# Performance work log

Hardware: AMD Instinct MI355X
Metric: run time of the kernel (lower is better)

The kernel has to match this reference:

```python
import jax, jax.numpy as jnp
import numpy as np

TAU_1 = 100.0


def setup_inputs() -> dict:
    key = jax.random.key(0)
    z = jax.random.normal(key, (8192, 512), dtype=jnp.float32)
    return {"z": z}


def reference(z) -> jnp.ndarray:
    # InfoNCE_l2 variant: log E_{i!=j}[ exp(-||z_i - z_j||^2 / tau_1) ]
    N = z.shape[0]
    sq = jnp.sum(z * z, axis=1)                      # [N]
    # squared euclidean distances: ||zi||^2 + ||zj||^2 - 2 zi.zj, clamped at 0
    D = jnp.maximum(sq[:, None] + sq[None, :] - 2.0 * (z @ z.T), 0.0)  # [N, N]
    E = jnp.exp(-D / TAU_1)
    # zero out the diagonal, average over the N*(N-1) off-diagonal entries
    off_diag_sum = jnp.sum(E) - jnp.sum(jnp.diagonal(E))
    mean_off = off_diag_sum / (N * (N - 1))
    return jnp.log(mean_off)
```

## Files before the change

kernel.cpp:

```cpp
#include <hip/hip_runtime.h>
#include <hip/hip_bf16.h>

#define NROWS 8192
#define KDIM  512
#define NT    64
#define NBLK  (NT*(NT+1)/2)
#define SCL1  0x7F7F7F7F
#define STRIP_BYTES (32 * KDIM)
#define C2    0.0144269504f

typedef __attribute__((ext_vector_type(16))) float f32x16;
typedef __attribute__((ext_vector_type(4))) int i32x4;
typedef __attribute__((ext_vector_type(8))) int i32x8;

__device__ __forceinline__ i32x8 mk_op(i32x4 lo, i32x4 hi) {
    i32x8 r;
    r[0] = lo[0]; r[1] = lo[1]; r[2] = lo[2]; r[3] = lo[3];
    r[4] = hi[0]; r[5] = hi[1]; r[6] = hi[2]; r[7] = hi[3];
    return r;
}

__global__ __launch_bounds__(256) void prep_kernel(const float* __restrict__ z,
                                                   unsigned char* __restrict__ zb2,
                                                   float* __restrict__ nq) {
    int wave = threadIdx.x >> 6, lane = threadIdx.x & 63;
    int row = blockIdx.x * 4 + wave;
    const float* zr = z + (size_t)row * KDIM + lane * 8;
    float4 v0 = *(const float4*)zr;
    float4 v1 = *(const float4*)(zr + 4);
    float vals[8] = {v0.x, v0.y, v0.z, v0.w, v1.x, v1.y, v1.z, v1.w};
    float s = 0.f;
#pragma unroll
    for (int i = 0; i < 8; ++i) s += vals[i] * vals[i];
    int lo = __builtin_amdgcn_cvt_pk_fp8_f32(vals[0], vals[1], 0, false);
    lo     = __builtin_amdgcn_cvt_pk_fp8_f32(vals[2], vals[3], lo, true);
    int hi = __builtin_amdgcn_cvt_pk_fp8_f32(vals[4], vals[5], 0, false);
    hi     = __builtin_amdgcn_cvt_pk_fp8_f32(vals[6], vals[7], hi, true);
    int2 pk; pk.x = lo; pk.y = hi;
    int strip = row >> 5, lr = row & 31;
    size_t addr = (size_t)strip * STRIP_BYTES + (lane >> 3) * 2048 +
                  ((lane >> 1) & 3) * 512 + lr * 16 + (lane & 1) * 8;
    *(int2*)(zb2 + addr) = pk;
#pragma unroll
    for (int off = 32; off; off >>= 1) s += __shfl_down(s, off);
    if (lane == 0) nq[row] = -C2 * s;
}

__global__ __launch_bounds__(256, 2) void gram_kernel(const unsigned char* __restrict__ zb2,
                                                      const float* __restrict__ nq,
                                                      float* __restrict__ part) {
    __shared__ float wsum[4];

    int tid = threadIdx.x;
    int wave = tid >> 6, lane = tid & 63;
    int ln31 = lane & 31, kh = lane >> 5;
    int wm = wave >> 1, wn = wave & 1;

    int rem = blockIdx.x, bi = 0;
    while (rem >= NT - bi) { rem -= NT - bi; ++bi; }
    int bj = bi + rem;
    int rot = blockIdx.x & 7;

    int sA = bi * 4 + wm * 2;
    int sB = bj * 4 + wn * 2;
    int laneOff = kh * 1024 + ln31 * 16;
    const unsigned char* pA0 = zb2 + (size_t)sA * STRIP_BYTES + laneOff;
    const unsigned char* pA1 = pA0 + STRIP_BYTES;
    const unsigned char* pB0 = zb2 + (size_t)sB * STRIP_BYTES + laneOff;
    const unsigned char* pB1 = pB0 + STRIP_BYTES;

    f32x16 accf[2][2];
#pragma unroll
    for (int mi = 0; mi < 2; ++mi)
#pragma unroll
        for (int ni = 0; ni < 2; ++ni)
#pragma unroll
            for (int r = 0; r < 16; ++r) accf[mi][ni][r] = 0.f;

#pragma unroll
    for (int h = 0; h < 2; ++h) {
        i32x4 Av[16], Bv[16];
#pragma unroll
        for (int ks = 0; ks < 4; ++ks) {
            int off = (((h * 4 + ks + rot) & 7)) * 2048;
            Av[ks * 4 + 0] = *(const i32x4*)(pA0 + off);
            Av[ks * 4 + 1] = *(const i32x4*)(pA0 + off + 512);
            Av[ks * 4 + 2] = *(const i32x4*)(pA1 + off);
            Av[ks * 4 + 3] = *(const i32x4*)(pA1 + off + 512);
            Bv[ks * 4 + 0] = *(const i32x4*)(pB0 + off);
            Bv[ks * 4 + 1] = *(const i32x4*)(pB0 + off + 512);
            Bv[ks * 4 + 2] = *(const i32x4*)(pB1 + off);
            Bv[ks * 4 + 3] = *(const i32x4*)(pB1 + off + 512);
        }
#pragma unroll
        for (int ks = 0; ks < 4; ++ks) {
            i32x8 a0 = mk_op(Av[ks * 4 + 0], Av[ks * 4 + 1]);
            i32x8 a1 = mk_op(Av[ks * 4 + 2], Av[ks * 4 + 3]);
            i32x8 b0 = mk_op(Bv[ks * 4 + 0], Bv[ks * 4 + 1]);
            i32x8 b1 = mk_op(Bv[ks * 4 + 2], Bv[ks * 4 + 3]);
            accf[0][0] = __builtin_amdgcn_mfma_scale_f32_32x32x64_f8f6f4(a0, b0, accf[0][0], 0, 0, 0, SCL1, 0, SCL1);
            accf[0][1] = __builtin_amdgcn_mfma_scale_f32_32x32x64_f8f6f4(a0, b1, accf[0][1], 0, 0, 0, SCL1, 0, SCL1);
            accf[1][0] = __builtin_amdgcn_mfma_scale_f32_32x32x64_f8f6f4(a1, b0, accf[1][0], 0, 0, 0, SCL1, 0, SCL1);
            accf[1][1] = __builtin_amdgcn_mfma_scale_f32_32x32x64_f8f6f4(a1, b1, accf[1][1], 0, 0, 0, SCL1, 0, SCL1);
        }
    }

    int rowBase = bi * 128 + wm * 64;
    int colBase = bj * 128 + wn * 64;
    float nqj[2] = { nq[colBase + ln31], nq[colBase + 32 + ln31] };

    float local = 0.f;
    if (bi != bj) {
#pragma unroll
        for (int mi = 0; mi < 2; ++mi) {
#pragma unroll
            for (int reg = 0; reg < 16; ++reg) {
                int rowf = (reg & 3) + 8 * (reg >> 2) + 4 * kh;
                float nqi = nq[rowBase + mi * 32 + rowf];
#pragma unroll
                for (int ni = 0; ni < 2; ++ni) {
                    float arg = fmaf(accf[mi][ni][reg], 2.f * C2, nqi + nqj[ni]);
                    local += __builtin_exp2f(fminf(arg, 0.f));
                }
            }
        }
    } else {
#pragma unroll
        for (int mi = 0; mi < 2; ++mi) {
#pragma unroll
            for (int reg = 0; reg < 16; ++reg) {
                int rowf = (reg & 3) + 8 * (reg >> 2) + 4 * kh;
                int gi = rowBase + mi * 32 + rowf;
                float nqi = nq[gi];
#pragma unroll
                for (int ni = 0; ni < 2; ++ni) {
                    int gj = colBase + ni * 32 + ln31;
                    float arg = fmaf(accf[mi][ni][reg], 2.f * C2, nqi + nqj[ni]);
                    float e = __builtin_exp2f(fminf(arg, 0.f));
                    local += (gi < gj) ? e : 0.f;
                }
            }
        }
    }

#pragma unroll
    for (int off = 32; off; off >>= 1) local += __shfl_down(local, off);
    if (lane == 0) wsum[wave] = local;
    __syncthreads();
    if (tid == 0) part[blockIdx.x] = wsum[0] + wsum[1] + wsum[2] + wsum[3];
}

__global__ __launch_bounds__(256) void reduce_kernel(const float* __restrict__ part,
                                                     float* __restrict__ out) {
    int tid = threadIdx.x;
    int wave = tid >> 6, lane = tid & 63;
    float s = 0.f;
    for (int i = tid; i < NBLK; i += 256) s += part[i];
#pragma unroll
    for (int off = 32; off; off >>= 1) s += __shfl_down(s, off);
    __shared__ float w[4];
    if (lane == 0) w[wave] = s;
    __syncthreads();
    if (tid == 0) {
        float total = 2.f * (w[0] + w[1] + w[2] + w[3]);
        out[0] = logf(total / ((float)NROWS * (float)(NROWS - 1)));
    }
}

extern "C" void kernel_launch(void* const* d_in, const int* in_sizes, int n_in,
                              void* d_out, int out_size, void* d_ws, size_t ws_size,
                              hipStream_t stream) {
    const float* z = (const float*)d_in[0];
    float* out = (float*)d_out;
    unsigned char* zb2 = (unsigned char*)d_ws;
    float* nq = (float*)((char*)d_ws + (size_t)NROWS * KDIM);
    float* part = nq + NROWS;

    prep_kernel<<<NROWS / 4, 256, 0, stream>>>(z, zb2, nq);
    gram_kernel<<<NBLK, 256, 0, stream>>>(zb2, nq, part);
    reduce_kernel<<<1, 256, 0, stream>>>(part, out);
}
```

Before: 91.84 us.

## Fuse prep, gram and reduce into one persistent cooperative kernel

Replaces three launches with a single cooperative kernel of 512 persistent blocks. The blocks first quantize rows to fp8 and compute norms, then grid-sync, loop over triangular tiles, grid-sync again, and let block 0 do the final reduction. The K loop is split into four smaller halves to cut register pressure. This removes launch gaps and tail effects, but adds two grid-wide barriers and the cost of cooperative launch, and the fixed grid may balance work unevenly across the 2080 tiles.

```diff
diff --git a/kernel.cpp b/kernel.cpp
--- a/kernel.cpp
+++ b/kernel.cpp
@@ -1,10 +1,14 @@
 #include <hip/hip_runtime.h>
+#include <hip/hip_cooperative_groups.h>
 #include <hip/hip_bf16.h>
+
+namespace cg = cooperative_groups;
 
 #define NROWS 8192
 #define KDIM  512
 #define NT    64
 #define NBLK  (NT*(NT+1)/2)
+#define GRID  512
 #define SCL1  0x7F7F7F7F
 #define STRIP_BYTES (32 * KDIM)
 #define C2    0.0144269504f
@@ -20,124 +24,129 @@
     return r;
 }
 
-__global__ __launch_bounds__(256) void prep_kernel(const float* __restrict__ z,
-                                                   unsigned char* __restrict__ zb2,
-                                                   float* __restrict__ nq) {
-    int wave = threadIdx.x >> 6, lane = threadIdx.x & 63;
-    int row = blockIdx.x * 4 + wave;
-    const float* zr = z + (size_t)row * KDIM + lane * 8;
-    float4 v0 = *(const float4*)zr;
-    float4 v1 = *(const float4*)(zr + 4);
-    float vals[8] = {v0.x, v0.y, v0.z, v0.w, v1.x, v1.y, v1.z, v1.w};
-    float s = 0.f;
-#pragma unroll
-    for (int i = 0; i < 8; ++i) s += vals[i] * vals[i];
-    int lo = __builtin_amdgcn_cvt_pk_fp8_f32(vals[0], vals[1], 0, false);
-    lo     = __builtin_amdgcn_cvt_pk_fp8_f32(vals[2], vals[3], lo, true);
-    int hi = __builtin_amdgcn_cvt_pk_fp8_f32(vals[4], vals[5], 0, false);
-    hi     = __builtin_amdgcn_cvt_pk_fp8_f32(vals[6], vals[7], hi, true);
-    int2 pk; pk.x = lo; pk.y = hi;
-    int strip = row >> 5, lr = row & 31;
-    size_t addr = (size_t)strip * STRIP_BYTES + (lane >> 3) * 2048 +
-                  ((lane >> 1) & 3) * 512 + lr * 16 + (lane & 1) * 8;
-    *(int2*)(zb2 + addr) = pk;
-#pragma unroll
-    for (int off = 32; off; off >>= 1) s += __shfl_down(s, off);
-    if (lane == 0) nq[row] = -C2 * s;
-}
-
-__global__ __launch_bounds__(256, 2) void gram_kernel(const unsigned char* __restrict__ zb2,
-                                                      const float* __restrict__ nq,
-                                                      float* __restrict__ part) {
+__global__ __launch_bounds__(256, 2) void fused_kernel(const float* __restrict__ z,
+                                                       unsigned char* __restrict__ zb2,
+                                                       float* __restrict__ nq,
+                                                       float* __restrict__ part,
+                                                       float* __restrict__ out) {
+    cg::grid_group gg = cg::this_grid();
     __shared__ float wsum[4];
 
     int tid = threadIdx.x;
     int wave = tid >> 6, lane = tid & 63;
+
+#pragma unroll
+    for (int rr = 0; rr < 4; ++rr) {
+        int row = blockIdx.x * 16 + wave * 4 + rr;
+        const float* zr = z + (size_t)row * KDIM + lane * 8;
+        float4 v0 = *(const float4*)zr;
+        float4 v1 = *(const float4*)(zr + 4);
+        float vals[8] = {v0.x, v0.y, v0.z, v0.w, v1.x, v1.y, v1.z, v1.w};
+        float s = 0.f;
+#pragma unroll
+        for (int i = 0; i < 8; ++i) s += vals[i] * vals[i];
+        int lo = __builtin_amdgcn_cvt_pk_fp8_f32(vals[0], vals[1], 0, false);
+        lo     = __builtin_amdgcn_cvt_pk_fp8_f32(vals[2], vals[3], lo, true);
+        int hi = __builtin_amdgcn_cvt_pk_fp8_f32(vals[4], vals[5], 0, false);
+        hi     = __builtin_amdgcn_cvt_pk_fp8_f32(vals[6], vals[7], hi, true);
+        int2 pk; pk.x = lo; pk.y = hi;
+        int strip = row >> 5, lr = row & 31;
+        size_t addr = (size_t)strip * STRIP_BYTES + (lane >> 3) * 2048 +
+                      ((lane >> 1) & 3) * 512 + lr * 16 + (lane & 1) * 8;
+        *(int2*)(zb2 + addr) = pk;
+#pragma unroll
+        for (int off = 32; off; off >>= 1) s += __shfl_down(s, off);
+        if (lane == 0) nq[row] = -C2 * s;
+    }
+
+    __threadfence();
+    gg.sync();
+
     int ln31 = lane & 31, kh = lane >> 5;
     int wm = wave >> 1, wn = wave & 1;
+    int laneOff = kh * 1024 + ln31 * 16;
 
-    int rem = blockIdx.x, bi = 0;
-    while (rem >= NT - bi) { rem -= NT - bi; ++bi; }
-    int bj = bi + rem;
-    int rot = blockIdx.x & 7;
+    float local = 0.f;
+    for (int t = blockIdx.x; t < NBLK; t += GRID) {
+        int rem = t, bi = 0;
+        while (rem >= NT - bi) { rem -= NT - bi; ++bi; }
+        int bj = bi + rem;
+        int rot = t & 7;
 
-    int sA = bi * 4 + wm * 2;
-    int sB = bj * 4 + wn * 2;
-    int laneOff = kh * 1024 + ln31 * 16;
-    const unsigned char* pA0 = zb2 + (size_t)sA * STRIP_BYTES + laneOff;
-    const unsigned char* pA1 = pA0 + STRIP_BYTES;
-    const unsigned char* pB0 = zb2 + (size_t)sB * STRIP_BYTES + laneOff;
-    const unsigned char* pB1 = pB0 + STRIP_BYTES;
+        const unsigned char* pA0 = zb2 + (size_t)(bi * 4 + wm * 2) * STRIP_BYTES + laneOff;
+        const unsigned char* pA1 = pA0 + STRIP_BYTES;
+        const unsigned char* pB0 = zb2 + (size_t)(bj * 4 + wn * 2) * STRIP_BYTES + laneOff;
+        const unsigned char* pB1 = pB0 + STRIP_BYTES;
 
-    f32x16 accf[2][2];
+        f32x16 accf[2][2];
 #pragma unroll
-    for (int mi = 0; mi < 2; ++mi)
+        for (int mi = 0; mi < 2; ++mi)
 #pragma unroll
-        for (int ni = 0; ni < 2; ++ni)
+            for (int ni = 0; ni < 2; ++ni)
 #pragma unroll
-            for (int r = 0; r < 16; ++r) accf[mi][ni][r] = 0.f;
+                for (int r = 0; r < 16; ++r) accf[mi][ni][r] = 0.f;
 
 #pragma unroll
-    for (int h = 0; h < 2; ++h) {
-        i32x4 Av[16], Bv[16];
+        for (int h = 0; h < 4; ++h) {
+            i32x4 Av[8], Bv[8];
 #pragma unroll
-        for (int ks = 0; ks < 4; ++ks) {
-            int off = (((h * 4 + ks + rot) & 7)) * 2048;
-            Av[ks * 4 + 0] = *(const i32x4*)(pA0 + off);
-            Av[ks * 4 + 1] = *(const i32x4*)(pA0 + off + 512);
-            Av[ks * 4 + 2] = *(const i32x4*)(pA1 + off);
-            Av[ks * 4 + 3] = *(const i32x4*)(pA1 + off + 512);
-            Bv[ks * 4 + 0] = *(const i32x4*)(pB0 + off);
-            Bv[ks * 4 + 1] = *(const i32x4*)(pB0 + off + 512);
-            Bv[ks * 4 + 2] = *(const i32x4*)(pB1 + off);
-            Bv[ks * 4 + 3] = *(const i32x4*)(pB1 + off + 512);
+            for (int ks = 0; ks < 2; ++ks) {
+                int off = ((h * 2 + ks + rot) & 7) * 2048;
+                Av[ks * 4 + 0] = *(const i32x4*)(pA0 + off);
+                Av[ks * 4 + 1] = *(const i32x4*)(pA0 + off + 512);
+                Av[ks * 4 + 2] = *(const i32x4*)(pA1 + off);
+                Av[ks * 4 + 3] = *(const i32x4*)(pA1 + off + 512);
+                Bv[ks * 4 + 0] = *(const i32x4*)(pB0 + off);
+                Bv[ks * 4 + 1] = *(const i32x4*)(pB0 + off + 512);
+                Bv[ks * 4 + 2] = *(const i32x4*)(pB1 + off);
+                Bv[ks * 4 + 3] = *(const i32x4*)(pB1 + off + 512);
+            }
+#pragma unroll
+            for (int ks = 0; ks < 2; ++ks) {
+                i32x8 a0 = mk_op(Av[ks * 4 + 0], Av[ks * 4 + 1]);
+                i32x8 a1 = mk_op(Av[ks * 4 + 2], Av[ks * 4 + 3]);
+                i32x8 b0 = mk_op(Bv[ks * 4 + 0], Bv[ks * 4 + 1]);
+                i32x8 b1 = mk_op(Bv[ks * 4 + 2], Bv[ks * 4 + 3]);
+                accf[0][0] = __builtin_amdgcn_mfma_scale_f32_32x32x64_f8f6f4(a0, b0, accf[0][0], 0, 0, 0, SCL1, 0, SCL1);
+                accf[0][1] = __builtin_amdgcn_mfma_scale_f32_32x32x64_f8f6f4(a0, b1, accf[0][1], 0, 0, 0, SCL1, 0, SCL1);
+                accf[1][0] = __builtin_amdgcn_mfma_scale_f32_32x32x64_f8f6f4(a1, b0, accf[1][0], 0, 0, 0, SCL1, 0, SCL1);
+                accf[1][1] = __builtin_amdgcn_mfma_scale_f32_32x32x64_f8f6f4(a1, b1, accf[1][1], 0, 0, 0, SCL1, 0, SCL1);
+            }
         }
+
+        int rowBase = bi * 128 + wm * 64;
+        int colBase = bj * 128 + wn * 64;
+        float nqj[2] = { nq[colBase + ln31], nq[colBase + 32 + ln31] };
+
+        if (bi != bj) {
 #pragma unroll
-        for (int ks = 0; ks < 4; ++ks) {
-            i32x8 a0 = mk_op(Av[ks * 4 + 0], Av[ks * 4 + 1]);
-            i32x8 a1 = mk_op(Av[ks * 4 + 2], Av[ks * 4 + 3]);
-            i32x8 b0 = mk_op(Bv[ks * 4 + 0], Bv[ks * 4 + 1]);
-            i32x8 b1 = mk_op(Bv[ks * 4 + 2], Bv[ks * 4 + 3]);
-            accf[0][0] = __builtin_amdgcn_mfma_scale_f32_32x32x64_f8f6f4(a0, b0, accf[0][0], 0, 0, 0, SCL1, 0, SCL1);
-            accf[0][1] = __builtin_amdgcn_mfma_scale_f32_32x32x64_f8f6f4(a0, b1, accf[0][1], 0, 0, 0, SCL1, 0, SCL1);
-            accf[1][0] = __builtin_amdgcn_mfma_scale_f32_32x32x64_f8f6f4(a1, b0, accf[1][0], 0, 0, 0, SCL1, 0, SCL1);
-            accf[1][1] = __builtin_amdgcn_mfma_scale_f32_32x32x64_f8f6f4(a1, b1, accf[1][1], 0, 0, 0, SCL1, 0, SCL1);
-        }
-    }
-
-    int rowBase = bi * 128 + wm * 64;
-    int colBase = bj * 128 + wn * 64;
-    float nqj[2] = { nq[colBase + ln31], nq[colBase + 32 + ln31] };
-
-    float local = 0.f;
-    if (bi != bj) {
+            for (int mi = 0; mi < 2; ++mi) {
 #pragma unroll
-        for (int mi = 0; mi < 2; ++mi) {
+                for (int reg = 0; reg < 16; ++reg) {
+                    int rowf = (reg & 3) + 8 * (reg >> 2) + 4 * kh;
+                    float nqi = nq[rowBase + mi * 32 + rowf];
 #pragma unroll
-            for (int reg = 0; reg < 16; ++reg) {
-                int rowf = (reg & 3) + 8 * (reg >> 2) + 4 * kh;
-                float nqi = nq[rowBase + mi * 32 + rowf];
-#pragma unroll
-                for (int ni = 0; ni < 2; ++ni) {
-                    float arg = fmaf(accf[mi][ni][reg], 2.f * C2, nqi + nqj[ni]);
-                    local += __builtin_exp2f(fminf(arg, 0.f));
+                    for (int ni = 0; ni < 2; ++ni) {
+                        float arg = fmaf(accf[mi][ni][reg], 2.f * C2, nqi + nqj[ni]);
+                        local += __builtin_exp2f(fminf(arg, 0.f));
+                    }
                 }
             }
-        }
-    } else {
+        } else {
 #pragma unroll
-        for (int mi = 0; mi < 2; ++mi) {
+            for (int mi = 0; mi < 2; ++mi) {
 #pragma unroll
-            for (int reg = 0; reg < 16; ++reg) {
-                int rowf = (reg & 3) + 8 * (reg >> 2) + 4 * kh;
-                int gi = rowBase + mi * 32 + rowf;
-                float nqi = nq[gi];
+                for (int reg = 0; reg < 16; ++reg) {
+                    int rowf = (reg & 3) + 8 * (reg >> 2) + 4 * kh;
+                    int gi = rowBase + mi * 32 + rowf;
+                    float nqi = nq[gi];
 #pragma unroll
-                for (int ni = 0; ni < 2; ++ni) {
-                    int gj = colBase + ni * 32 + ln31;
-                    float arg = fmaf(accf[mi][ni][reg], 2.f * C2, nqi + nqj[ni]);
-                    float e = __builtin_exp2f(fminf(arg, 0.f));
-                    local += (gi < gj) ? e : 0.f;
+                    for (int ni = 0; ni < 2; ++ni) {
+                        int gj = colBase + ni * 32 + ln31;
+                        float arg = fmaf(accf[mi][ni][reg], 2.f * C2, nqi + nqj[ni]);
+                        float e = __builtin_exp2f(fminf(arg, 0.f));
+                        local += (gi < gj) ? e : 0.f;
+                    }
                 }
             }
         }
@@ -148,22 +157,22 @@
     if (lane == 0) wsum[wave] = local;
     __syncthreads();
     if (tid == 0) part[blockIdx.x] = wsum[0] + wsum[1] + wsum[2] + wsum[3];
-}
 
-__global__ __launch_bounds__(256) void reduce_kernel(const float* __restrict__ part,
-                                                     float* __restrict__ out) {
-    int tid = threadIdx.x;
-    int wave = tid >> 6, lane = tid & 63;
-    float s = 0.f;
-    for (int i = tid; i < NBLK; i += 256) s += part[i];
+    __threadfence();
+    gg.sync();
+
+    if (blockIdx.x == 0) {
+        float s = 0.f;
+        for (int i = tid; i < GRID; i += 256) s += part[i];
 #pragma unroll
-    for (int off = 32; off; off >>= 1) s += __shfl_down(s, off);
-    __shared__ float w[4];
-    if (lane == 0) w[wave] = s;
-    __syncthreads();
-    if (tid == 0) {
-        float total = 2.f * (w[0] + w[1] + w[2] + w[3]);
-        out[0] = logf(total / ((float)NROWS * (float)(NROWS - 1)));
+        for (int off = 32; off; off >>= 1) s += __shfl_down(s, off);
+        __syncthreads();
+        if (lane == 0) wsum[wave] = s;
+        __syncthreads();
+        if (tid == 0) {
+            float total = 2.f * (wsum[0] + wsum[1] + wsum[2] + wsum[3]);
+            out[0] = logf(total / ((float)NROWS * (float)(NROWS - 1)));
+        }
     }
 }
 
@@ -176,7 +185,7 @@
     float* nq = (float*)((char*)d_ws + (size_t)NROWS * KDIM);
     float* part = nq + NROWS;
 
-    prep_kernel<<<NROWS / 4, 256, 0, stream>>>(z, zb2, nq);
-    gram_kernel<<<NBLK, 256, 0, stream>>>(zb2, nq, part);
-    reduce_kernel<<<1, 256, 0, stream>>>(part, out);
+    void* args[] = { (void*)&z, (void*)&zb2, (void*)&nq, (void*)&part, (void*)&out };
+    hipLaunchCooperativeKernel((const void*)fused_kernel, dim3(GRID), dim3(256),
+                               args, 0, stream);
 }
```

New measurement: 322.8 us. 251% more time.

## Enlarge gram tiles to 256x256 with 4x4 MFMA per wave and skip lower diagonal waves

Applied to the files above, without the earlier changes.

Doubles the block tile from 128x128 to 256x256, so each wave computes a 128x128 sub-tile with a 4x4 grid of FP8 MFMA accumulators. This raises arithmetic intensity per byte loaded and cuts the number of upper-triangle blocks from 2080 to 528. Waves in diagonal blocks whose sub-tile lies wholly below the diagonal now skip all work. The cost is a much larger register footprint, with 256 accumulator floats per lane and launch bounds dropped to one block per CU, plus fewer blocks to spread across the CUs.

```diff
diff --git a/kernel.cpp b/kernel.cpp
--- a/kernel.cpp
+++ b/kernel.cpp
@@ -3,8 +3,8 @@
 
 #define NROWS 8192
 #define KDIM  512
-#define NT    64
-#define NBLK  (NT*(NT+1)/2)
+#define NT2   32
+#define NBLK2 (NT2*(NT2+1)/2)
 #define SCL1  0x7F7F7F7F
 #define STRIP_BYTES (32 * KDIM)
 #define C2    0.0144269504f
@@ -46,7 +46,7 @@
     if (lane == 0) nq[row] = -C2 * s;
 }
 
-__global__ __launch_bounds__(256, 2) void gram_kernel(const unsigned char* __restrict__ zb2,
+__global__ __launch_bounds__(256, 1) void gram_kernel(const unsigned char* __restrict__ zb2,
                                                       const float* __restrict__ nq,
                                                       float* __restrict__ part) {
     __shared__ float wsum[4];
@@ -57,87 +57,83 @@
     int wm = wave >> 1, wn = wave & 1;
 
     int rem = blockIdx.x, bi = 0;
-    while (rem >= NT - bi) { rem -= NT - bi; ++bi; }
+    while (rem >= NT2 - bi) { rem -= NT2 - bi; ++bi; }
     int bj = bi + rem;
     int rot = blockIdx.x & 7;
 
-    int sA = bi * 4 + wm * 2;
-    int sB = bj * 4 + wn * 2;
-    int laneOff = kh * 1024 + ln31 * 16;
-    const unsigned char* pA0 = zb2 + (size_t)sA * STRIP_BYTES + laneOff;
-    const unsigned char* pA1 = pA0 + STRIP_BYTES;
-    const unsigned char* pB0 = zb2 + (size_t)sB * STRIP_BYTES + laneOff;
-    const unsigned char* pB1 = pB0 + STRIP_BYTES;
+    float local = 0.f;
+    bool skip = (bi == bj) && (wm > wn);
 
-    f32x16 accf[2][2];
+    if (!skip) {
+        int laneOff = kh * 1024 + ln31 * 16;
+        const unsigned char* pA[4];
+        const unsigned char* pB[4];
 #pragma unroll
-    for (int mi = 0; mi < 2; ++mi)
+        for (int s = 0; s < 4; ++s) {
+            pA[s] = zb2 + (size_t)(bi * 8 + wm * 4 + s) * STRIP_BYTES + laneOff;
+            pB[s] = zb2 + (size_t)(bj * 8 + wn * 4 + s) * STRIP_BYTES + laneOff;
+        }
+
+        f32x16 accf[4][4];
 #pragma unroll
-        for (int ni = 0; ni < 2; ++ni)
+        for (int mi = 0; mi < 4; ++mi)
 #pragma unroll
-            for (int r = 0; r < 16; ++r) accf[mi][ni][r] = 0.f;
+            for (int ni = 0; ni < 4; ++ni)
+#pragma unroll
+                for (int r = 0; r < 16; ++r) accf[mi][ni][r] = 0.f;
 
+        for (int ks = 0; ks < 8; ++ks) {
+            int off = ((ks + rot) & 7) * 2048;
+            i32x8 a[4], b[4];
 #pragma unroll
-    for (int h = 0; h < 2; ++h) {
-        i32x4 Av[16], Bv[16];
+            for (int s = 0; s < 4; ++s) {
+                a[s] = mk_op(*(const i32x4*)(pA[s] + off), *(const i32x4*)(pA[s] + off + 512));
+                b[s] = mk_op(*(const i32x4*)(pB[s] + off), *(const i32x4*)(pB[s] + off + 512));
+            }
 #pragma unroll
-        for (int ks = 0; ks < 4; ++ks) {
-            int off = (((h * 4 + ks + rot) & 7)) * 2048;
-            Av[ks * 4 + 0] = *(const i32x4*)(pA0 + off);
-            Av[ks * 4 + 1] = *(const i32x4*)(pA0 + off + 512);
-            Av[ks * 4 + 2] = *(const i32x4*)(pA1 + off);
-            Av[ks * 4 + 3] = *(const i32x4*)(pA1 + off + 512);
-            Bv[ks * 4 + 0] = *(const i32x4*)(pB0 + off);
-            Bv[ks * 4 + 1] = *(const i32x4*)(pB0 + off + 512);
-            Bv[ks * 4 + 2] = *(const i32x4*)(pB1 + off);
-            Bv[ks * 4 + 3] = *(const i32x4*)(pB1 + off + 512);
+            for (int mi = 0; mi < 4; ++mi)
+#pragma unroll
+                for (int ni = 0; ni < 4; ++ni)
+                    accf[mi][ni] = __builtin_amdgcn_mfma_scale_f32_32x32x64_f8f6f4(
+                        a[mi], b[ni], accf[mi][ni], 0, 0, 0, SCL1, 0, SCL1);
         }
+
+        int rowBase = bi * 256 + wm * 128;
+        int colBase = bj * 256 + wn * 128;
+        float nqj[4];
 #pragma unroll
-        for (int ks = 0; ks < 4; ++ks) {
-            i32x8 a0 = mk_op(Av[ks * 4 + 0], Av[ks * 4 + 1]);
-            i32x8 a1 = mk_op(Av[ks * 4 + 2], Av[ks * 4 + 3]);
-            i32x8 b0 = mk_op(Bv[ks * 4 + 0], Bv[ks * 4 + 1]);
-            i32x8 b1 = mk_op(Bv[ks * 4 + 2], Bv[ks * 4 + 3]);
-            accf[0][0] = __builtin_amdgcn_mfma_scale_f32_32x32x64_f8f6f4(a0, b0, accf[0][0], 0, 0, 0, SCL1, 0, SCL1);
-            accf[0][1] = __builtin_amdgcn_mfma_scale_f32_32x32x64_f8f6f4(a0, b1, accf[0][1], 0, 0, 0, SCL1, 0, SCL1);
-            accf[1][0] = __builtin_amdgcn_mfma_scale_f32_32x32x64_f8f6f4(a1, b0, accf[1][0], 0, 0, 0, SCL1, 0, SCL1);
-            accf[1][1] = __builtin_amdgcn_mfma_scale_f32_32x32x64_f8f6f4(a1, b1, accf[1][1], 0, 0, 0, SCL1, 0, SCL1);
-        }
-    }
+        for (int ni = 0; ni < 4; ++ni) nqj[ni] = nq[colBase + ni * 32 + ln31];
 
-    int rowBase = bi * 128 + wm * 64;
-    int colBase = bj * 128 + wn * 64;
-    float nqj[2] = { nq[colBase + ln31], nq[colBase + 32 + ln31] };
-
-    float local = 0.f;
-    if (bi != bj) {
+        bool masked = (bi == bj) && (wm == wn);
+        if (!masked) {
 #pragma unroll
-        for (int mi = 0; mi < 2; ++mi) {
+            for (int mi = 0; mi < 4; ++mi) {
 #pragma unroll
-            for (int reg = 0; reg < 16; ++reg) {
-                int rowf = (reg & 3) + 8 * (reg >> 2) + 4 * kh;
-                float nqi = nq[rowBase + mi * 32 + rowf];
+                for (int reg = 0; reg < 16; ++reg) {
+                    int rowf = (reg & 3) + 8 * (reg >> 2) + 4 * kh;
+                    float nqi = nq[rowBase + mi * 32 + rowf];
 #pragma unroll
-                for (int ni = 0; ni < 2; ++ni) {
-                    float arg = fmaf(accf[mi][ni][reg], 2.f * C2, nqi + nqj[ni]);
-                    local += __builtin_exp2f(fminf(arg, 0.f));
+                    for (int ni = 0; ni < 4; ++ni) {
+                        float arg = fmaf(accf[mi][ni][reg], 2.f * C2, nqi + nqj[ni]);
+                        local += __builtin_exp2f(fminf(arg, 0.f));
+                    }
                 }
             }
-        }
-    } else {
+        } else {
 #pragma unroll
-        for (int mi = 0; mi < 2; ++mi) {
+            for (int mi = 0; mi < 4; ++mi) {
 #pragma unroll
-            for (int reg = 0; reg < 16; ++reg) {
-                int rowf = (reg & 3) + 8 * (reg >> 2) + 4 * kh;
-                int gi = rowBase + mi * 32 + rowf;
-                float nqi = nq[gi];
+                for (int reg = 0; reg < 16; ++reg) {
+                    int rowf = (reg & 3) + 8 * (reg >> 2) + 4 * kh;
+                    int gi = rowBase + mi * 32 + rowf;
+                    float nqi = nq[gi];
 #pragma unroll
-                for (int ni = 0; ni < 2; ++ni) {
-                    int gj = colBase + ni * 32 + ln31;
-                    float arg = fmaf(accf[mi][ni][reg], 2.f * C2, nqi + nqj[ni]);
-                    float e = __builtin_exp2f(fminf(arg, 0.f));
-                    local += (gi < gj) ? e : 0.f;
+                    for (int ni = 0; ni < 4; ++ni) {
+                        int gj = colBase + ni * 32 + ln31;
+                        float arg = fmaf(accf[mi][ni][reg], 2.f * C2, nqi + nqj[ni]);
+                        float e = __builtin_exp2f(fminf(arg, 0.f));
+                        local += (gi < gj) ? e : 0.f;
+                    }
                 }
             }
         }
@@ -155,7 +151,7 @@
     int tid = threadIdx.x;
     int wave = tid >> 6, lane = tid & 63;
     float s = 0.f;
-    for (int i = tid; i < NBLK; i += 256) s += part[i];
+    for (int i = tid; i < NBLK2; i += 256) s += part[i];
 #pragma unroll
     for (int off = 32; off; off >>= 1) s += __shfl_down(s, off);
     __shared__ float w[4];
@@ -177,6 +173,6 @@
     float* part = nq + NROWS;
 
     prep_kernel<<<NROWS / 4, 256, 0, stream>>>(z, zb2, nq);
-    gram_kernel<<<NBLK, 256, 0, stream>>>(zb2, nq, part);
+    gram_kernel<<<NBLK2, 256, 0, stream>>>(zb2, nq, part);
     reduce_kernel<<<1, 256, 0, stream>>>(part, out);
 }
```

Measured after the change: 110.8 us. 20.6% more time.
